# Kernel tuning notes

Hardware: AMD Instinct MI355X
Metric: run time of the kernel (lower is better)

The kernel has to match this reference:

```python
import jax, jax.numpy as jnp
import numpy as np

GAMMA1 = 5.0
GAMMA2 = 5.0
ALPHA = 0.2
BETA = 1.0
K = 0.1
SEQ = 5

B = 16384
EMB = 64
ITEM_NUM = 200000
USER_NUM = 100000
CLUSTER = 64


def setup_inputs() -> dict:
    key = jax.random.key(0)
    ks = jax.random.split(key, 7)
    u = jax.random.randint(ks[0], (B,), 0, USER_NUM)
    X = jax.random.randint(ks[1], (B, SEQ), 0, ITEM_NUM + 1)
    y = jax.random.randint(ks[2], (B,), 0, ITEM_NUM + 1)
    item_emb = jax.random.normal(ks[3], (ITEM_NUM + 1, EMB), dtype=jnp.float32)
    user_emb = jax.random.normal(ks[4], (USER_NUM, EMB), dtype=jnp.float32)
    ae_raw = jax.random.normal(ks[5], (ITEM_NUM + 1, CLUSTER), dtype=jnp.float32)
    w_raw = jax.random.normal(ks[6], (CLUSTER, CLUSTER), dtype=jnp.float32)
    return {"u": u, "X": X, "y": y, "item_emb": item_emb,
            "user_emb": user_emb, "ae_raw": ae_raw, "w_raw": w_raw}


def reference(u, X, y, item_emb, user_emb, ae_raw, w_raw):
    # constructor preprocessing: _handle_ae / _filter_w
    ae = jax.nn.softmax(ae_raw * 10.0 * GAMMA1, axis=1)        # [I+1, C]
    w = jax.nn.softmax(w_raw * 100.0 * GAMMA2, axis=0)          # [C, C]
    # padding_idx=0 -> row 0 of item embedding is zero
    item_emb = item_emb.at[0].set(0.0)

    u_emb = user_emb[u]            # [B, E]
    X_emb = item_emb[X]            # [B, S, E]
    y_emb = item_emb[y]            # [B, E]

    # cluster affinity: ae[X] @ w @ ae[y]
    fac = jnp.einsum('bsc,cd,bd->bs', ae[X], w, ae[y])          # [B, S]

    # time attenuation: [0.6, 0.7, 0.8, 0.9, 1.0]
    time_factor = 1.0 - (SEQ - 1 - jnp.arange(SEQ, dtype=jnp.float32)) * K

    scores = (jnp.einsum('bse,be->bs', X_emb, y_emb)
              * BETA * jnp.exp(fac) * time_factor)              # [B, S]
    z = jax.nn.softmax(scores, axis=1)                          # [B, S]
    p = jnp.einsum('bse,bs->be', X_emb, z)                      # [B, E]
    p_u = p * ALPHA + u_emb                                     # [B, E]
    # diag(sigmoid(p_u @ y_emb.T)) == sigmoid(rowwise dot)
    return jax.nn.sigmoid(jnp.sum(p_u * y_emb, axis=-1))        # [B]
```

## Files before the change

kernel.cpp:

```cpp
#include <hip/hip_runtime.h>
#include <math.h>

#define SEQ 5
#define EMBC 64

typedef float4 f4;

template<int CTRL>
__device__ __forceinline__ float dpp_rot(float v) {
    return __int_as_float(__builtin_amdgcn_update_dpp(
        0, __float_as_int(v), CTRL, 0xF, 0xF, true));
}
__device__ __forceinline__ float sub_sum(float v) {
    v += dpp_rot<0x128>(v);
    v += dpp_rot<0x124>(v);
    v += dpp_rot<0x122>(v);
    v += dpp_rot<0x121>(v);
    return v;
}
__device__ __forceinline__ float sub_max(float v) {
    v = fmaxf(v, dpp_rot<0x128>(v));
    v = fmaxf(v, dpp_rot<0x124>(v));
    v = fmaxf(v, dpp_rot<0x122>(v));
    v = fmaxf(v, dpp_rot<0x121>(v));
    return v;
}
__device__ __forceinline__ float wave_max64(float v) {
    #pragma unroll
    for (int o = 32; o > 0; o >>= 1) v = fmaxf(v, __shfl_xor(v, o, 64));
    return v;
}
__device__ __forceinline__ float wave_sum64(float v) {
    #pragma unroll
    for (int o = 32; o > 0; o >>= 1) v += __shfl_xor(v, o, 64);
    return v;
}
__device__ __forceinline__ float dot4(f4 a, f4 b) {
    return fmaf(a.x, b.x, fmaf(a.y, b.y, fmaf(a.z, b.z, a.w * b.w)));
}
__device__ __forceinline__ f4 fma4(f4 a, float s, f4 c) {
    f4 r; r.x = fmaf(a.x, s, c.x); r.y = fmaf(a.y, s, c.y);
          r.z = fmaf(a.z, s, c.z); r.w = fmaf(a.w, s, c.w); return r;
}
__device__ __forceinline__ f4 sub_softmax(f4 a, float scale) {
    a.x *= scale; a.y *= scale; a.z *= scale; a.w *= scale;
    const float m = sub_max(fmaxf(fmaxf(a.x, a.y), fmaxf(a.z, a.w)));
    f4 e; e.x = __expf(a.x - m); e.y = __expf(a.y - m);
          e.z = __expf(a.z - m); e.w = __expf(a.w - m);
    const float inv = 1.0f / sub_sum(((e.x + e.y) + (e.z + e.w)));
    e.x *= inv; e.y *= inv; e.z *= inv; e.w *= inv;
    return e;
}

__global__ __launch_bounds__(64) void wprep_kernel(
    const float* __restrict__ w_raw, float* __restrict__ wT)
{
    const int d = blockIdx.x;
    const int c = threadIdx.x;
    float x = w_raw[c * EMBC + d] * 500.0f;
    const float m = wave_max64(x);
    const float e = __expf(x - m);
    const float s = wave_sum64(e);
    wT[d * EMBC + c] = e / s;
}

__global__ __launch_bounds__(256) void rumc_main(
    const int* __restrict__ u_idx, const int* __restrict__ X_idx,
    const int* __restrict__ y_idx,
    const float* __restrict__ item_emb, const float* __restrict__ user_emb,
    const float* __restrict__ ae_raw, const float* __restrict__ wT,
    float* __restrict__ out, int B)
{
    __shared__ f4 s_w[EMBC * 16];
    __shared__ f4 s_ae[16 * 16];

    const int t = threadIdx.x;

    #pragma unroll
    for (int i = 0; i < 4; ++i)
        s_w[t + 256 * i] = ((const f4*)wT)[t + 256 * i];

    const int wave = t >> 6;
    const int lane = t & 63;
    const int sub  = lane >> 4;
    const int sl   = lane & 15;
    const int g    = wave * 4 + sub;

    int b = blockIdx.x * 16 + g;
    const bool live = (b < B);
    if (!live) b = B - 1;

    __syncthreads();

    const int yi = y_idx[b];
    const int ui = u_idx[b];
    int xi[SEQ];
    #pragma unroll
    for (int s = 0; s < SEQ; ++s) xi[s] = X_idx[b * SEQ + s];

    const f4* __restrict__ item4 = (const f4*)item_emb;
    const f4* __restrict__ user4 = (const f4*)user_emb;
    const f4* __restrict__ ae4   = (const f4*)ae_raw;

    f4 aey = ae4[yi * 16 + sl];
    f4 ax[SEQ];
    #pragma unroll
    for (int s = 0; s < SEQ; ++s) ax[s] = ae4[xi[s] * 16 + sl];
    f4 ye = item4[yi * 16 + sl];
    f4 xe[SEQ];
    #pragma unroll
    for (int s = 0; s < SEQ; ++s) xe[s] = item4[xi[s] * 16 + sl];
    f4 ue = user4[ui * 16 + sl];

    if (yi == 0) { ye.x = ye.y = ye.z = ye.w = 0.0f; }
    #pragma unroll
    for (int s = 0; s < SEQ; ++s)
        if (xi[s] == 0) { xe[s].x = xe[s].y = xe[s].z = xe[s].w = 0.0f; }

    aey = sub_softmax(aey, 50.0f);
    s_ae[g * 16 + sl] = aey;

    f4 v; v.x = v.y = v.z = v.w = 0.0f;
    #pragma unroll
    for (int dd = 0; dd < 16; ++dd) {
        const f4 a  = s_ae[g * 16 + dd];
        const f4 w0 = s_w[(4 * dd + 0) * 16 + sl];
        const f4 w1 = s_w[(4 * dd + 1) * 16 + sl];
        const f4 w2 = s_w[(4 * dd + 2) * 16 + sl];
        const f4 w3 = s_w[(4 * dd + 3) * 16 + sl];
        v = fma4(w0, a.x, v);
        v = fma4(w1, a.y, v);
        v = fma4(w2, a.z, v);
        v = fma4(w3, a.w, v);
    }

    float sc[SEQ];
    #pragma unroll
    for (int s = 0; s < SEQ; ++s) {
        const f4 a = sub_softmax(ax[s], 50.0f);
        const float fac = sub_sum(dot4(a, v));
        const float dot = sub_sum(dot4(xe[s], ye));
        const float tf = 1.0f - (float)(SEQ - 1 - s) * 0.1f;
        sc[s] = dot * __expf(fac) * tf;
    }

    float ms = sc[0];
    #pragma unroll
    for (int s = 1; s < SEQ; ++s) ms = fmaxf(ms, sc[s]);
    float Z = 0.0f;
    #pragma unroll
    for (int s = 0; s < SEQ; ++s) { sc[s] = __expf(sc[s] - ms); Z += sc[s]; }
    const float invZ = 1.0f / Z;

    f4 p; p.x = p.y = p.z = p.w = 0.0f;
    #pragma unroll
    for (int s = 0; s < SEQ; ++s) p = fma4(xe[s], sc[s] * invZ, p);
    const f4 pu = fma4(p, 0.2f, ue);
    const float fin = sub_sum(dot4(pu, ye));
    if (live && sl == 0)
        out[b] = 1.0f / (1.0f + __expf(-fin));
}

extern "C" void kernel_launch(void* const* d_in, const int* in_sizes, int n_in,
                              void* d_out, int out_size, void* d_ws, size_t ws_size,
                              hipStream_t stream) {
    const int*   u        = (const int*)d_in[0];
    const int*   X        = (const int*)d_in[1];
    const int*   y        = (const int*)d_in[2];
    const float* item_emb = (const float*)d_in[3];
    const float* user_emb = (const float*)d_in[4];
    const float* ae_raw   = (const float*)d_in[5];
    const float* w_raw    = (const float*)d_in[6];
    float*       out      = (float*)d_out;
    float*       wT       = (float*)d_ws;

    const int B = in_sizes[0];
    const int grid = (B + 15) / 16;

    wprep_kernel<<<EMBC, EMBC, 0, stream>>>(w_raw, wT);
    rumc_main<<<grid, 256, 0, stream>>>(u, X, y, item_emb, user_emb,
                                        ae_raw, wT, out, B);
}
```

Baseline: 141.0 us.

## Drop shared-memory W staging; split matvec across subgroups with cross-lane reduction

Removes the 16KB shared-memory copy of the cluster weight matrix and the block barrier. Each 16-lane subgroup now reads a quarter of W directly from global/L2 and computes partial products for all four batch rows in its wave. The partials are then combined with xor shuffles, so each W element is loaded once per wave instead of once per row. The launch bound is raised to four blocks per CU. This trades LDS traffic and the barrier for extra shuffle instructions, global loads that rely on cache hits, and more register pressure.

```diff
diff --git a/kernel.cpp b/kernel.cpp
--- a/kernel.cpp
+++ b/kernel.cpp
@@ -41,6 +41,15 @@
 __device__ __forceinline__ f4 fma4(f4 a, float s, f4 c) {
     f4 r; r.x = fmaf(a.x, s, c.x); r.y = fmaf(a.y, s, c.y);
           r.z = fmaf(a.z, s, c.z); r.w = fmaf(a.w, s, c.w); return r;
+}
+__device__ __forceinline__ f4 add4(f4 a, f4 b) {
+    f4 r; r.x = a.x + b.x; r.y = a.y + b.y;
+          r.z = a.z + b.z; r.w = a.w + b.w; return r;
+}
+__device__ __forceinline__ f4 shfl_xor4(f4 v, int mask) {
+    f4 r; r.x = __shfl_xor(v.x, mask, 64); r.y = __shfl_xor(v.y, mask, 64);
+          r.z = __shfl_xor(v.z, mask, 64); r.w = __shfl_xor(v.w, mask, 64);
+    return r;
 }
 __device__ __forceinline__ f4 sub_softmax(f4 a, float scale) {
     a.x *= scale; a.y *= scale; a.z *= scale; a.w *= scale;
@@ -64,22 +73,16 @@
     wT[d * EMBC + c] = e / s;
 }
 
-__global__ __launch_bounds__(256) void rumc_main(
+__global__ __launch_bounds__(256, 4) void rumc_main(
     const int* __restrict__ u_idx, const int* __restrict__ X_idx,
     const int* __restrict__ y_idx,
     const float* __restrict__ item_emb, const float* __restrict__ user_emb,
     const float* __restrict__ ae_raw, const float* __restrict__ wT,
     float* __restrict__ out, int B)
 {
-    __shared__ f4 s_w[EMBC * 16];
     __shared__ f4 s_ae[16 * 16];
 
-    const int t = threadIdx.x;
-
-    #pragma unroll
-    for (int i = 0; i < 4; ++i)
-        s_w[t + 256 * i] = ((const f4*)wT)[t + 256 * i];
-
+    const int t    = threadIdx.x;
     const int wave = t >> 6;
     const int lane = t & 63;
     const int sub  = lane >> 4;
@@ -90,8 +93,6 @@
     const bool live = (b < B);
     if (!live) b = B - 1;
 
-    __syncthreads();
-
     const int yi = y_idx[b];
     const int ui = u_idx[b];
     int xi[SEQ];
@@ -101,6 +102,7 @@
     const f4* __restrict__ item4 = (const f4*)item_emb;
     const f4* __restrict__ user4 = (const f4*)user_emb;
     const f4* __restrict__ ae4   = (const f4*)ae_raw;
+    const f4* __restrict__ wT4   = (const f4*)wT;
 
     f4 aey = ae4[yi * 16 + sl];
     f4 ax[SEQ];
@@ -120,19 +122,35 @@
     aey = sub_softmax(aey, 50.0f);
     s_ae[g * 16 + sl] = aey;
 
-    f4 v; v.x = v.y = v.z = v.w = 0.0f;
-    #pragma unroll
-    for (int dd = 0; dd < 16; ++dd) {
-        const f4 a  = s_ae[g * 16 + dd];
-        const f4 w0 = s_w[(4 * dd + 0) * 16 + sl];
-        const f4 w1 = s_w[(4 * dd + 1) * 16 + sl];
-        const f4 w2 = s_w[(4 * dd + 2) * 16 + sl];
-        const f4 w3 = s_w[(4 * dd + 3) * 16 + sl];
-        v = fma4(w0, a.x, v);
-        v = fma4(w1, a.y, v);
-        v = fma4(w2, a.z, v);
-        v = fma4(w3, a.w, v);
+    f4 vp[4];
+    #pragma unroll
+    for (int bb = 0; bb < 4; ++bb) vp[bb].x = vp[bb].y = vp[bb].z = vp[bb].w = 0.0f;
+
+    #pragma unroll
+    for (int jc = 0; jc < 4; ++jc) {
+        const int d0 = 16 * sub + 4 * jc;
+        const f4 w0 = wT4[(d0 + 0) * 16 + sl];
+        const f4 w1 = wT4[(d0 + 1) * 16 + sl];
+        const f4 w2 = wT4[(d0 + 2) * 16 + sl];
+        const f4 w3 = wT4[(d0 + 3) * 16 + sl];
+        #pragma unroll
+        for (int bb = 0; bb < 4; ++bb) {
+            const f4 a = s_ae[(wave * 4 + bb) * 16 + 4 * sub + jc];
+            vp[bb] = fma4(w0, a.x, vp[bb]);
+            vp[bb] = fma4(w1, a.y, vp[bb]);
+            vp[bb] = fma4(w2, a.z, vp[bb]);
+            vp[bb] = fma4(w3, a.w, vp[bb]);
+        }
     }
+    #pragma unroll
+    for (int bb = 0; bb < 4; ++bb) {
+        vp[bb] = add4(vp[bb], shfl_xor4(vp[bb], 16));
+        vp[bb] = add4(vp[bb], shfl_xor4(vp[bb], 32));
+    }
+    f4 v = vp[0];
+    if (sub == 1) v = vp[1];
+    if (sub == 2) v = vp[2];
+    if (sub == 3) v = vp[3];
 
     float sc[SEQ];
     #pragma unroll
```

After: 153.3 us. 1.09x slower.
